# Performance work log

Hardware: AMD Instinct MI355X
Metric: run time of the kernel (lower is better)

## Reference

```python
import jax, jax.numpy as jnp
import numpy as np

# Circuit structure constants (HCLT-style tensorized probabilistic circuit)
V = 128      # num_vars
M = 256      # num_latents (input nodes per variable)
C = 64       # num categories per variable
B = 256      # batch size
L = 4        # number of inner (prod, sum) layer pairs
N = 32768    # sum nodes per inner layer
K = 4        # sum-node fanin (children product elements per sum node)
A = 2        # product-node arity
E = N * K    # product elements per layer
NUM_INPUT = V * M


def setup_inputs() -> dict:
    key = jax.random.key(0)
    k1, k2, k3, k4 = jax.random.split(key, 4)
    inputs = jax.random.randint(k1, (B, V), 0, C)                          # [B, V] categorical data
    input_logits = jax.random.normal(k2, (NUM_INPUT, C), dtype=jnp.float32)  # per input-node categorical logits
    sum_logits = jax.random.normal(k3, (L, N, K), dtype=jnp.float32)         # per sum-node edge logits (grouped softmax)
    root_logits = jax.random.normal(k4, (N,), dtype=jnp.float32)             # root sum-node edge logits
    # Irregular child index structure: prod element e in layer l gathers A children
    # from any node computed so far (dummy node 0 excluded, indices >= 1).
    rng = np.random.default_rng(0)
    base = 1 + NUM_INPUT
    child = np.stack([rng.integers(1, base + l * N, size=(E, A)) for l in range(L)], axis=0)
    prod_child_ids = jnp.asarray(child, dtype=jnp.int32)                    # [L, E, A]
    return {"inputs": inputs, "input_logits": input_logits, "sum_logits": sum_logits,
            "root_logits": root_logits, "prod_child_ids": prod_child_ids}


def reference(inputs, input_logits, sum_logits, root_logits, prod_child_ids):
    # --- input layer: node_mars for input nodes = log p(x_{vid(n)} | node n) ---
    logp = jax.nn.log_softmax(input_logits, axis=-1)            # [VM, C]
    vids = jnp.arange(NUM_INPUT) // M                           # variable id per input node
    cats = inputs[:, vids].T                                    # [VM, B] category index per (node, batch)
    in_mars = jnp.take_along_axis(logp, cats, axis=1)           # [VM, B]
    # node 0 is the dummy node with log-marginal 0.0 (as in the original buffer init)
    node_buf = jnp.concatenate([jnp.zeros((1, B), dtype=in_mars.dtype), in_mars], axis=0)
    # --- inner layers: alternating ProdLayer (gather+add) and SumLayer (softmax params + logsumexp) ---
    for l in range(L):
        ch = node_buf[prod_child_ids[l]]                        # [E, A, B] irregular gather
        elem = ch.sum(axis=1)                                   # element_mars: [E, B]
        logw = jax.nn.log_softmax(sum_logits[l], axis=-1)       # per-node grouped softmax: [N, K]
        nodes = jax.nn.logsumexp(elem.reshape(N, K, B) + logw[:, :, None], axis=1)  # [N, B]
        node_buf = jnp.concatenate([node_buf, nodes], axis=0)
    # --- root sum node ---
    rw = jax.nn.log_softmax(root_logits)                        # [N]
    lls = jax.nn.logsumexp(node_buf[-N:] + rw[:, None], axis=0) # [B]
    return lls[:, None]                                         # [B, num_roots=1]
```

## Files before the change

kernel.cpp:

```cpp
#include <hip/hip_runtime.h>
#include <math.h>

#define V 128
#define M 256
#define CAT 64
#define B 256
#define LAYERS 4
#define N 32768
#define K 4
#define AR 2
#define E (N * K)
#define NUM_INPUT (V * M)
#define BASE (1 + NUM_INPUT)
#define TOTAL_ROWS (BASE + LAYERS * N)
#define L3N 32
#define NPART (N / L3N)
#define R1BLK 32

typedef _Float16 half8 __attribute__((ext_vector_type(8)));
typedef _Float16 half4 __attribute__((ext_vector_type(4)));
typedef float float8_t __attribute__((ext_vector_type(8)));

#define OFF_IN 5.2f
__device__ __forceinline__ float layer_off(int l) {
    const float o[4] = {11.4f, 23.5f, 47.5f, 95.5f};
    return o[l];
}
__device__ __forceinline__ float row_off(int row) {
    return (row < BASE) ? OFF_IN : layer_off((row - BASE) >> 15);
}

__global__ __launch_bounds__(256) void input_layer_kernel(
    const int* __restrict__ inputs,
    const float* __restrict__ input_logits,
    _Float16* __restrict__ buf)
{
    __shared__ float lg[4][CAT];
    __shared__ int cats[B];
    __shared__ float lzs[4];
    const int t = threadIdx.x;
    const int n0 = blockIdx.x * 4;

    lg[t >> 6][t & 63] = input_logits[(size_t)n0 * CAT + t];
    cats[t] = inputs[t * V + (n0 >> 8)];
    __syncthreads();

    const int w = t >> 6;
    const int l = t & 63;
    float x = lg[w][l];
    float m = x;
    #pragma unroll
    for (int off = 32; off >= 1; off >>= 1) m = fmaxf(m, __shfl_xor(m, off));
    float s = __expf(x - m);
    #pragma unroll
    for (int off = 32; off >= 1; off >>= 1) s += __shfl_xor(s, off);
    if (l == 0) lzs[w] = m + __logf(s);
    __syncthreads();

    const float logZ = lzs[w];
    half4 r;
    #pragma unroll
    for (int j = 0; j < 4; ++j) {
        const int c = cats[4 * l + j];
        r[j] = (_Float16)(lg[w][c] - logZ + OFF_IN);
    }
    ((half4*)buf)[(size_t)(1 + n0 + w) * (B / 4) + l] = r;

    if (blockIdx.x == 0 && t < B / 4) {
        half4 z;
        z[0] = z[1] = z[2] = z[3] = (_Float16)OFF_IN;
        ((half4*)buf)[t] = z;
    }
}

__global__ __launch_bounds__(256) void layer_kernel(
    const int* __restrict__ child,
    const float* __restrict__ slog,
    _Float16* __restrict__ buf,
    int out_row0, int layer)
{
    __shared__ int ch[8][K * AR];
    __shared__ float w[8][K];
    const int t = threadIdx.x;
    const int i0 = blockIdx.x * 8;

    if (t < 64) ((int*)ch)[t] = child[(size_t)i0 * (K * AR) + t];
    __syncthreads();

    if (t < 32) {
        const float x = slog[(size_t)i0 * K + t];
        float mm = fmaxf(x, __shfl_xor(x, 1));
        mm = fmaxf(mm, __shfl_xor(mm, 2));
        float e = __expf(x - mm);
        float ss = e + __shfl_xor(e, 1);
        ss += __shfl_xor(ss, 2);
        const float lz = mm + __logf(ss);
        const int j = t >> 2, k = t & 3;
        w[j][k] = x - lz - row_off(ch[j][2 * k]) - row_off(ch[j][2 * k + 1])
                  + layer_off(layer);
    }
    __syncthreads();

    const int g = t >> 5;
    const int l = t & 31;
    const half8* bufv = (const half8*)buf;

    float8_t v[K];
    #pragma unroll
    for (int k = 0; k < K; ++k) {
        const half8 a = bufv[ch[g][2 * k]     * (B / 8) + l];
        const half8 b = bufv[ch[g][2 * k + 1] * (B / 8) + l];
        v[k] = __builtin_convertvector(a, float8_t) +
               __builtin_convertvector(b, float8_t) + w[g][k];
    }

    half8 r;
    #pragma unroll
    for (int j = 0; j < 8; ++j) {
        const float mm = fmaxf(fmaxf(v[0][j], v[1][j]), fmaxf(v[2][j], v[3][j]));
        const float ss = __expf(v[0][j] - mm) + __expf(v[1][j] - mm) +
                         __expf(v[2][j] - mm) + __expf(v[3][j] - mm);
        r[j] = (_Float16)(mm + __logf(ss));
    }
    ((half8*)buf)[(out_row0 + i0 + g) * (B / 8) + l] = r;
}

__global__ __launch_bounds__(1024) void layer3_root_kernel(
    const int* __restrict__ child,
    const float* __restrict__ slog,
    const _Float16* __restrict__ buf,
    const float* __restrict__ rlog,
    float* __restrict__ pm, float* __restrict__ ps)
{
    __shared__ int ch[L3N][K * AR];
    __shared__ float w[L3N][K];
    __shared__ float rl[L3N];
    __shared__ float vmat[B][L3N + 1];
    const int t = threadIdx.x;
    const int i0 = blockIdx.x * L3N;
    const float off3 = layer_off(3);

    if (t < L3N * 8) ((int*)ch)[t] = child[(size_t)i0 * (K * AR) + t];
    if (t >= 512 && t < 512 + L3N) rl[t - 512] = rlog[i0 + (t - 512)];
    __syncthreads();

    if (t < L3N * 4) {
        const float x = slog[(size_t)i0 * K + t];
        float mm = fmaxf(x, __shfl_xor(x, 1));
        mm = fmaxf(mm, __shfl_xor(mm, 2));
        float e = __expf(x - mm);
        float ss = e + __shfl_xor(e, 1);
        ss += __shfl_xor(ss, 2);
        const float lz = mm + __logf(ss);
        const int j = t >> 2, k = t & 3;
        w[j][k] = x - lz - row_off(ch[j][2 * k]) - row_off(ch[j][2 * k + 1])
                  + off3;
    }
    __syncthreads();

    const int g = t >> 5;
    const int l = t & 31;

    const half8* bufv = (const half8*)buf;
    float8_t v[K];
    #pragma unroll
    for (int k = 0; k < K; ++k) {
        const half8 a = bufv[ch[g][2 * k]     * (B / 8) + l];
        const half8 b = bufv[ch[g][2 * k + 1] * (B / 8) + l];
        v[k] = __builtin_convertvector(a, float8_t) +
               __builtin_convertvector(b, float8_t) + w[g][k];
    }

    const float radd = rl[g] - off3;
    #pragma unroll
    for (int j = 0; j < 8; ++j) {
        const float mm = fmaxf(fmaxf(v[0][j], v[1][j]), fmaxf(v[2][j], v[3][j]));
        const float ss = __expf(v[0][j] - mm) + __expf(v[1][j] - mm) +
                         __expf(v[2][j] - mm) + __expf(v[3][j] - mm);
        vmat[8 * l + j][g] = mm + __logf(ss) + radd;
    }
    __syncthreads();

    if (t < B) {
        float m = -INFINITY;
        #pragma unroll
        for (int q = 0; q < L3N; ++q) m = fmaxf(m, vmat[t][q]);
        float s = 0.0f;
        #pragma unroll
        for (int q = 0; q < L3N; ++q) s += __expf(vmat[t][q] - m);
        pm[blockIdx.x * B + t] = m;
        ps[blockIdx.x * B + t] = s;
    }
}

__global__ __launch_bounds__(256) void root_reduce1(
    const float* __restrict__ pm, const float* __restrict__ ps,
    float* __restrict__ pm2, float* __restrict__ ps2)
{
    const int j = blockIdx.x;
    const int c = threadIdx.x;
    const int Q = NPART / R1BLK;
    const int p0 = j * Q;

    float m = -INFINITY;
    #pragma unroll 8
    for (int q = 0; q < Q; ++q) m = fmaxf(m, pm[(p0 + q) * B + c]);
    float s = 0.0f;
    #pragma unroll 8
    for (int q = 0; q < Q; ++q)
        s += ps[(p0 + q) * B + c] * __expf(pm[(p0 + q) * B + c] - m);
    pm2[j * B + c] = m;
    ps2[j * B + c] = s;
}

__global__ __launch_bounds__(256) void root_combine_kernel(
    const float* __restrict__ rlog,
    const float* __restrict__ pm2, const float* __restrict__ ps2,
    float* __restrict__ out)
{
    __shared__ float red[256];
    const int t = threadIdx.x;

    float a0 = -INFINITY, a1 = -INFINITY, a2 = -INFINITY, a3 = -INFINITY;
    #pragma unroll 4
    for (int n = t; n < N; n += 1024) {
        a0 = fmaxf(a0, rlog[n]);
        a1 = fmaxf(a1, rlog[n + 256]);
        a2 = fmaxf(a2, rlog[n + 512]);
        a3 = fmaxf(a3, rlog[n + 768]);
    }
    red[t] = fmaxf(fmaxf(a0, a1), fmaxf(a2, a3));
    __syncthreads();
    for (int off = 128; off >= 1; off >>= 1) {
        if (t < off) red[t] = fmaxf(red[t], red[t + off]);
        __syncthreads();
    }
    const float gm = red[0];
    __syncthreads();

    float b0 = 0.f, b1 = 0.f, b2 = 0.f, b3 = 0.f;
    #pragma unroll 4
    for (int n = t; n < N; n += 1024) {
        b0 += __expf(rlog[n]       - gm);
        b1 += __expf(rlog[n + 256] - gm);
        b2 += __expf(rlog[n + 512] - gm);
        b3 += __expf(rlog[n + 768] - gm);
    }
    red[t] = (b0 + b1) + (b2 + b3);
    __syncthreads();
    for (int off = 128; off >= 1; off >>= 1) {
        if (t < off) red[t] += red[t + off];
        __syncthreads();
    }
    const float logZ = gm + __logf(red[0]);

    float m = -INFINITY;
    #pragma unroll 8
    for (int p = 0; p < R1BLK; ++p) m = fmaxf(m, pm2[p * B + t]);
    float s = 0.0f;
    #pragma unroll 8
    for (int p = 0; p < R1BLK; ++p)
        s += ps2[p * B + t] * __expf(pm2[p * B + t] - m);
    out[t] = m + __logf(s) - logZ;
}

extern "C" void kernel_launch(void* const* d_in, const int* in_sizes, int n_in,
                              void* d_out, int out_size, void* d_ws, size_t ws_size,
                              hipStream_t stream) {
    const int*   inputs       = (const int*)d_in[0];
    const float* input_logits = (const float*)d_in[1];
    const float* sum_logits   = (const float*)d_in[2];
    const float* root_logits  = (const float*)d_in[3];
    const int*   child        = (const int*)d_in[4];
    float* out = (float*)d_out;

    _Float16* buf = (_Float16*)d_ws;
    float* pm  = (float*)(buf + (size_t)TOTAL_ROWS * B);
    float* ps  = pm  + (size_t)NPART * B;
    float* pm2 = ps  + (size_t)NPART * B;
    float* ps2 = pm2 + (size_t)R1BLK * B;

    input_layer_kernel<<<NUM_INPUT / 4, 256, 0, stream>>>(inputs, input_logits, buf);

    for (int l = 0; l < LAYERS - 1; ++l) {
        layer_kernel<<<N / 8, 256, 0, stream>>>(
            child + (size_t)l * E * AR,
            sum_logits + (size_t)l * N * K,
            buf,
            BASE + l * N, l);
    }

    layer3_root_kernel<<<NPART, 1024, 0, stream>>>(
        child + (size_t)(LAYERS - 1) * E * AR,
        sum_logits + (size_t)(LAYERS - 1) * N * K,
        buf, root_logits, pm, ps);

    root_reduce1<<<R1BLK, 256, 0, stream>>>(pm, ps, pm2, ps2);
    root_combine_kernel<<<1, 256, 0, stream>>>(root_logits, pm2, ps2, out);
}
```

Measured before the change: 127.9 us.

## Rebuild input-node marginals on the fly from a compact log-prob table

The input stage no longer writes the full fp16 matrix of input-node marginals (one row per input node, times the batch). It now writes only a per-node fp16 log-softmax table (64 categories) and a byte-packed category matrix per variable. When a child index points to an input node, the layer kernels fetch the compact table row and the category bytes, then pick each batch element's value with a ds_bpermute lookup inside each 32-lane group. The aim is to cut the large input write and the 512-byte-per-row reads of input children. In exchange it adds branchy per-child decoding, cross-lane permute instructions and more registers in the gather kernels.

```diff
diff --git a/kernel.cpp b/kernel.cpp
--- a/kernel.cpp
+++ b/kernel.cpp
@@ -1,81 +1,104 @@
 #include <hip/hip_runtime.h>
 #include <math.h>
+#include <stdint.h>
 
 #define V 128
 #define M 256
 #define CAT 64
 #define B 256
 #define LAYERS 4
-#define N 32768
 #define K 4
 #define AR 2
-#define E (N * K)
+#define NNODES 32768
+#define E (NNODES * K)
 #define NUM_INPUT (V * M)
 #define BASE (1 + NUM_INPUT)
-#define TOTAL_ROWS (BASE + LAYERS * N)
+#define TOTAL_ROWS (BASE + LAYERS * NNODES)
 #define L3N 32
-#define NPART (N / L3N)
+#define NPART (NNODES / L3N)
 #define R1BLK 32
 
 typedef _Float16 half8 __attribute__((ext_vector_type(8)));
-typedef _Float16 half4 __attribute__((ext_vector_type(4)));
 typedef float float8_t __attribute__((ext_vector_type(8)));
 
 #define OFF_IN 5.2f
 __device__ __forceinline__ float layer_off(int l) {
-    const float o[4] = {11.4f, 23.5f, 47.5f, 95.5f};
-    return o[l];
+    return (l == 0) ? 11.4f : (l == 1) ? 23.5f : (l == 2) ? 47.5f : 95.5f;
 }
 __device__ __forceinline__ float row_off(int row) {
-    return (row < BASE) ? OFF_IN : layer_off((row - BASE) >> 15);
-}
-
-__global__ __launch_bounds__(256) void input_layer_kernel(
+    if (row < BASE) return OFF_IN;
+    return layer_off((row - BASE) >> 15);
+}
+
+__global__ __launch_bounds__(256) void input_prep_kernel(
     const int* __restrict__ inputs,
     const float* __restrict__ input_logits,
-    _Float16* __restrict__ buf)
-{
-    __shared__ float lg[4][CAT];
-    __shared__ int cats[B];
-    __shared__ float lzs[4];
+    _Float16* __restrict__ logp16,
+    unsigned char* __restrict__ cats)
+{
     const int t = threadIdx.x;
     const int n0 = blockIdx.x * 4;
-
-    lg[t >> 6][t & 63] = input_logits[(size_t)n0 * CAT + t];
-    cats[t] = inputs[t * V + (n0 >> 8)];
-    __syncthreads();
-
     const int w = t >> 6;
     const int l = t & 63;
-    float x = lg[w][l];
+    const int n = n0 + w;
+
+    const float x = input_logits[(size_t)n * CAT + l];
     float m = x;
     #pragma unroll
     for (int off = 32; off >= 1; off >>= 1) m = fmaxf(m, __shfl_xor(m, off));
     float s = __expf(x - m);
     #pragma unroll
     for (int off = 32; off >= 1; off >>= 1) s += __shfl_xor(s, off);
-    if (l == 0) lzs[w] = m + __logf(s);
-    __syncthreads();
-
-    const float logZ = lzs[w];
-    half4 r;
-    #pragma unroll
-    for (int j = 0; j < 4; ++j) {
-        const int c = cats[4 * l + j];
-        r[j] = (_Float16)(lg[w][c] - logZ + OFF_IN);
-    }
-    ((half4*)buf)[(size_t)(1 + n0 + w) * (B / 4) + l] = r;
-
-    if (blockIdx.x == 0 && t < B / 4) {
-        half4 z;
-        z[0] = z[1] = z[2] = z[3] = (_Float16)OFF_IN;
-        ((half4*)buf)[t] = z;
-    }
+    const float logZ = m + __logf(s);
+
+    logp16[(size_t)n * 64 + l] = (_Float16)(x - logZ + OFF_IN);
+
+    if ((blockIdx.x & 63) == 0) {
+        const int v = blockIdx.x >> 6;
+        cats[(size_t)v * B + t] = (unsigned char)inputs[t * V + v];
+    }
+}
+
+#define STAGE_CHILD(r, lane, bufq, lpu, catsu, S0, S1, S2, S3)                \
+    if ((r) >= BASE) {                                                        \
+        const uint4 q = (bufq)[(size_t)(r) * 32 + (lane)];                    \
+        S0 = q.x; S1 = q.y; S2 = q.z; S3 = q.w;                               \
+    } else {                                                                  \
+        const int nn_ = (r) - 1;                                              \
+        S0 = (lpu)[(size_t)nn_ * 32 + (lane)];                                \
+        const uint64_t cc_ = (catsu)[(size_t)(nn_ >> 8) * 32 + (lane)];       \
+        S1 = (uint32_t)cc_; S2 = (uint32_t)(cc_ >> 32); S3 = 0u;              \
+    }
+
+__device__ __forceinline__ float8_t finish_child(
+    int r, int phys, uint32_t s0, uint32_t s1, uint32_t s2, uint32_t s3)
+{
+    float8_t val;
+    if (r >= BASE) {
+        union { uint32_t u[4]; half8 hh; } q;
+        q.u[0] = s0; q.u[1] = s1; q.u[2] = s2; q.u[3] = s3;
+        val = __builtin_convertvector(q.hh, float8_t);
+    } else {
+        const uint32_t bl = (uint32_t)(phys & 32);
+        #pragma unroll
+        for (int j = 0; j < 8; ++j) {
+            const uint32_t cb = (((j < 4) ? s1 : s2) >> (8 * (j & 3))) & 63u;
+            const uint32_t got = (uint32_t)__builtin_amdgcn_ds_bpermute(
+                (int)(((cb >> 1) | bl) << 2), (int)s0);
+            const unsigned short hb = (cb & 1u) ? (unsigned short)(got >> 16)
+                                                : (unsigned short)(got & 0xffffu);
+            union { unsigned short u; _Float16 h; } cv; cv.u = hb;
+            val[j] = (float)cv.h;
+        }
+    }
+    return val;
 }
 
 __global__ __launch_bounds__(256) void layer_kernel(
     const int* __restrict__ child,
     const float* __restrict__ slog,
+    const _Float16* __restrict__ logp16,
+    const unsigned char* __restrict__ cats,
     _Float16* __restrict__ buf,
     int out_row0, int layer)
 {
@@ -101,33 +124,43 @@
     }
     __syncthreads();
 
-    const int g = t >> 5;
-    const int l = t & 31;
-    const half8* bufv = (const half8*)buf;
+    const int g = t >> 5, lane = t & 31, phys = t & 63;
+    const uint4* bufq = (const uint4*)buf;
+    const uint32_t* lpu = (const uint32_t*)logp16;
+    const uint64_t* catsu = (const uint64_t*)cats;
+
+    uint32_t s0[8], s1[8], s2[8], s3[8];
+    #pragma unroll
+    for (int c = 0; c < 8; ++c) {
+        const int r = ch[g][c];
+        STAGE_CHILD(r, lane, bufq, lpu, catsu, s0[c], s1[c], s2[c], s3[c]);
+    }
 
     float8_t v[K];
     #pragma unroll
     for (int k = 0; k < K; ++k) {
-        const half8 a = bufv[ch[g][2 * k]     * (B / 8) + l];
-        const half8 b = bufv[ch[g][2 * k + 1] * (B / 8) + l];
-        v[k] = __builtin_convertvector(a, float8_t) +
-               __builtin_convertvector(b, float8_t) + w[g][k];
-    }
-
-    half8 r;
+        const int c0 = 2 * k, c1 = 2 * k + 1;
+        const float8_t a = finish_child(ch[g][c0], phys, s0[c0], s1[c0], s2[c0], s3[c0]);
+        const float8_t b = finish_child(ch[g][c1], phys, s0[c1], s1[c1], s2[c1], s3[c1]);
+        v[k] = a + b + w[g][k];
+    }
+
+    half8 r8;
     #pragma unroll
     for (int j = 0; j < 8; ++j) {
         const float mm = fmaxf(fmaxf(v[0][j], v[1][j]), fmaxf(v[2][j], v[3][j]));
         const float ss = __expf(v[0][j] - mm) + __expf(v[1][j] - mm) +
                          __expf(v[2][j] - mm) + __expf(v[3][j] - mm);
-        r[j] = (_Float16)(mm + __logf(ss));
-    }
-    ((half8*)buf)[(out_row0 + i0 + g) * (B / 8) + l] = r;
+        r8[j] = (_Float16)(mm + __logf(ss));
+    }
+    ((half8*)buf)[(size_t)(out_row0 + i0 + g) * 32 + lane] = r8;
 }
 
 __global__ __launch_bounds__(1024) void layer3_root_kernel(
     const int* __restrict__ child,
     const float* __restrict__ slog,
+    const _Float16* __restrict__ logp16,
+    const unsigned char* __restrict__ cats,
     const _Float16* __restrict__ buf,
     const float* __restrict__ rlog,
     float* __restrict__ pm, float* __restrict__ ps)
@@ -158,17 +191,25 @@
     }
     __syncthreads();
 
-    const int g = t >> 5;
-    const int l = t & 31;
-
-    const half8* bufv = (const half8*)buf;
+    const int g = t >> 5, lane = t & 31, phys = t & 63;
+    const uint4* bufq = (const uint4*)buf;
+    const uint32_t* lpu = (const uint32_t*)logp16;
+    const uint64_t* catsu = (const uint64_t*)cats;
+
+    uint32_t s0[8], s1[8], s2[8], s3[8];
+    #pragma unroll
+    for (int c = 0; c < 8; ++c) {
+        const int r = ch[g][c];
+        STAGE_CHILD(r, lane, bufq, lpu, catsu, s0[c], s1[c], s2[c], s3[c]);
+    }
+
     float8_t v[K];
     #pragma unroll
     for (int k = 0; k < K; ++k) {
-        const half8 a = bufv[ch[g][2 * k]     * (B / 8) + l];
-        const half8 b = bufv[ch[g][2 * k + 1] * (B / 8) + l];
-        v[k] = __builtin_convertvector(a, float8_t) +
-               __builtin_convertvector(b, float8_t) + w[g][k];
+        const int c0 = 2 * k, c1 = 2 * k + 1;
+        const float8_t a = finish_child(ch[g][c0], phys, s0[c0], s1[c0], s2[c0], s3[c0]);
+        const float8_t b = finish_child(ch[g][c1], phys, s0[c1], s1[c1], s2[c1], s3[c1]);
+        v[k] = a + b + w[g][k];
     }
 
     const float radd = rl[g] - off3;
@@ -177,7 +218,7 @@
         const float mm = fmaxf(fmaxf(v[0][j], v[1][j]), fmaxf(v[2][j], v[3][j]));
         const float ss = __expf(v[0][j] - mm) + __expf(v[1][j] - mm) +
                          __expf(v[2][j] - mm) + __expf(v[3][j] - mm);
-        vmat[8 * l + j][g] = mm + __logf(ss) + radd;
+        vmat[8 * lane + j][g] = mm + __logf(ss) + radd;
     }
     __syncthreads();
 
@@ -223,7 +264,7 @@
 
     float a0 = -INFINITY, a1 = -INFINITY, a2 = -INFINITY, a3 = -INFINITY;
     #pragma unroll 4
-    for (int n = t; n < N; n += 1024) {
+    for (int n = t; n < NNODES; n += 1024) {
         a0 = fmaxf(a0, rlog[n]);
         a1 = fmaxf(a1, rlog[n + 256]);
         a2 = fmaxf(a2, rlog[n + 512]);
@@ -240,7 +281,7 @@
 
     float b0 = 0.f, b1 = 0.f, b2 = 0.f, b3 = 0.f;
     #pragma unroll 4
-    for (int n = t; n < N; n += 1024) {
+    for (int n = t; n < NNODES; n += 1024) {
         b0 += __expf(rlog[n]       - gm);
         b1 += __expf(rlog[n + 256] - gm);
         b2 += __expf(rlog[n + 512] - gm);
@@ -275,25 +316,27 @@
     float* out = (float*)d_out;
 
     _Float16* buf = (_Float16*)d_ws;
-    float* pm  = (float*)(buf + (size_t)TOTAL_ROWS * B);
+    _Float16* logp16 = buf + (size_t)TOTAL_ROWS * B;
+    unsigned char* cats = (unsigned char*)(logp16 + (size_t)NUM_INPUT * 64);
+    float* pm  = (float*)(cats + (size_t)V * B);
     float* ps  = pm  + (size_t)NPART * B;
     float* pm2 = ps  + (size_t)NPART * B;
     float* ps2 = pm2 + (size_t)R1BLK * B;
 
-    input_layer_kernel<<<NUM_INPUT / 4, 256, 0, stream>>>(inputs, input_logits, buf);
+    input_prep_kernel<<<NUM_INPUT / 4, 256, 0, stream>>>(inputs, input_logits,
+                                                         logp16, cats);
 
     for (int l = 0; l < LAYERS - 1; ++l) {
-        layer_kernel<<<N / 8, 256, 0, stream>>>(
+        layer_kernel<<<NNODES / 8, 256, 0, stream>>>(
             child + (size_t)l * E * AR,
-            sum_logits + (size_t)l * N * K,
-            buf,
-            BASE + l * N, l);
+            sum_logits + (size_t)l * NNODES * K,
+            logp16, cats, buf, BASE + l * NNODES, l);
     }
 
     layer3_root_kernel<<<NPART, 1024, 0, stream>>>(
         child + (size_t)(LAYERS - 1) * E * AR,
-        sum_logits + (size_t)(LAYERS - 1) * N * K,
-        buf, root_logits, pm, ps);
+        sum_logits + (size_t)(LAYERS - 1) * NNODES * K,
+        logp16, cats, buf, root_logits, pm, ps);
 
     root_reduce1<<<R1BLK, 256, 0, stream>>>(pm, ps, pm2, ps2);
     root_combine_kernel<<<1, 256, 0, stream>>>(root_logits, pm2, ps2, out);
```

Measured after the change: 171.1 us. 33.7% more time.

## Partition batch columns across XCDs so each die's L2 caches a node-buffer slice

Applied to the files above, without the earlier changes.

Layer kernels now split the 256-wide batch into eight 32-column slices and assign the slice by blockIdx&7, relying on round-robin dispatch of blocks to the eight XCDs. Each XCD then gathers only its own 64-byte slice of every child row, so its private L2 holds one eighth of the fp16 node buffer instead of the whole thing. Each block handles 32 nodes with 8 threads per node and issues all eight child loads up front. The root layer kernel is rewritten to match, with 256-thread blocks writing partial max/sum per 32-column slice. The gathers become narrower 8-byte loads, and the locality gain depends on the hardware keeping its block-to-XCD mapping.

```diff
diff --git a/kernel.cpp b/kernel.cpp
--- a/kernel.cpp
+++ b/kernel.cpp
@@ -1,33 +1,32 @@
 #include <hip/hip_runtime.h>
 #include <math.h>
+#include <stdint.h>
 
 #define V 128
 #define M 256
 #define CAT 64
 #define B 256
 #define LAYERS 4
-#define N 32768
 #define K 4
 #define AR 2
-#define E (N * K)
+#define NNODES 32768
+#define E (NNODES * K)
 #define NUM_INPUT (V * M)
 #define BASE (1 + NUM_INPUT)
-#define TOTAL_ROWS (BASE + LAYERS * N)
-#define L3N 32
-#define NPART (N / L3N)
+#define TOTAL_ROWS (BASE + LAYERS * NNODES)
+#define NPART 1024
 #define R1BLK 32
 
-typedef _Float16 half8 __attribute__((ext_vector_type(8)));
 typedef _Float16 half4 __attribute__((ext_vector_type(4)));
-typedef float float8_t __attribute__((ext_vector_type(8)));
+typedef float float4v __attribute__((ext_vector_type(4)));
 
 #define OFF_IN 5.2f
 __device__ __forceinline__ float layer_off(int l) {
-    const float o[4] = {11.4f, 23.5f, 47.5f, 95.5f};
-    return o[l];
+    return (l == 0) ? 11.4f : (l == 1) ? 23.5f : (l == 2) ? 47.5f : 95.5f;
 }
 __device__ __forceinline__ float row_off(int row) {
-    return (row < BASE) ? OFF_IN : layer_off((row - BASE) >> 15);
+    if (row < BASE) return OFF_IN;
+    return layer_off((row - BASE) >> 15);
 }
 
 __global__ __launch_bounds__(256) void input_layer_kernel(
@@ -73,21 +72,23 @@
     }
 }
 
-__global__ __launch_bounds__(256) void layer_kernel(
+__global__ __launch_bounds__(256) void layer_kernel_xcd(
     const int* __restrict__ child,
     const float* __restrict__ slog,
     _Float16* __restrict__ buf,
     int out_row0, int layer)
 {
-    __shared__ int ch[8][K * AR];
-    __shared__ float w[8][K];
+    __shared__ int ch[32][K * AR];
+    __shared__ float w[32][K];
     const int t = threadIdx.x;
-    const int i0 = blockIdx.x * 8;
-
-    if (t < 64) ((int*)ch)[t] = child[(size_t)i0 * (K * AR) + t];
-    __syncthreads();
-
-    if (t < 32) {
+    const int xcd = blockIdx.x & 7;
+    const int chunk = blockIdx.x >> 3;
+    const int i0 = chunk * 32;
+
+    ((int*)ch)[t] = child[(size_t)i0 * (K * AR) + t];
+    __syncthreads();
+
+    if (t < 128) {
         const float x = slog[(size_t)i0 * K + t];
         float mm = fmaxf(x, __shfl_xor(x, 1));
         mm = fmaxf(mm, __shfl_xor(mm, 2));
@@ -101,50 +102,57 @@
     }
     __syncthreads();
 
-    const int g = t >> 5;
-    const int l = t & 31;
-    const half8* bufv = (const half8*)buf;
-
-    float8_t v[K];
+    const int g = t >> 3;
+    const int s = t & 7;
+    const int off = xcd * 8 + s;
+    const uint2* bufu = (const uint2*)buf;
+
+    uint2 st[8];
+    #pragma unroll
+    for (int c = 0; c < 8; ++c)
+        st[c] = bufu[(size_t)ch[g][c] * 64 + off];
+
+    float4v v[K];
     #pragma unroll
     for (int k = 0; k < K; ++k) {
-        const half8 a = bufv[ch[g][2 * k]     * (B / 8) + l];
-        const half8 b = bufv[ch[g][2 * k + 1] * (B / 8) + l];
-        v[k] = __builtin_convertvector(a, float8_t) +
-               __builtin_convertvector(b, float8_t) + w[g][k];
-    }
-
-    half8 r;
-    #pragma unroll
-    for (int j = 0; j < 8; ++j) {
+        union { uint2 u; half4 h; } ua, ub;
+        ua.u = st[2 * k]; ub.u = st[2 * k + 1];
+        v[k] = __builtin_convertvector(ua.h, float4v) +
+               __builtin_convertvector(ub.h, float4v) + w[g][k];
+    }
+
+    union { uint2 u; half4 h; } ro;
+    #pragma unroll
+    for (int j = 0; j < 4; ++j) {
         const float mm = fmaxf(fmaxf(v[0][j], v[1][j]), fmaxf(v[2][j], v[3][j]));
         const float ss = __expf(v[0][j] - mm) + __expf(v[1][j] - mm) +
                          __expf(v[2][j] - mm) + __expf(v[3][j] - mm);
-        r[j] = (_Float16)(mm + __logf(ss));
-    }
-    ((half8*)buf)[(out_row0 + i0 + g) * (B / 8) + l] = r;
-}
-
-__global__ __launch_bounds__(1024) void layer3_root_kernel(
+        ro.h[j] = (_Float16)(mm + __logf(ss));
+    }
+    ((uint2*)buf)[(size_t)(out_row0 + i0 + g) * 64 + off] = ro.u;
+}
+
+__global__ __launch_bounds__(256) void layer3_root_xcd(
     const int* __restrict__ child,
     const float* __restrict__ slog,
     const _Float16* __restrict__ buf,
     const float* __restrict__ rlog,
     float* __restrict__ pm, float* __restrict__ ps)
 {
-    __shared__ int ch[L3N][K * AR];
-    __shared__ float w[L3N][K];
-    __shared__ float rl[L3N];
-    __shared__ float vmat[B][L3N + 1];
+    __shared__ int ch[32][K * AR];
+    __shared__ float w[32][K];
+    __shared__ float rl[32];
+    __shared__ float vmat[32][33];
     const int t = threadIdx.x;
-    const int i0 = blockIdx.x * L3N;
+    const int xcd = blockIdx.x & 7;
+    const int chunk = blockIdx.x >> 3;
+    const int i0 = chunk * 32;
     const float off3 = layer_off(3);
 
-    if (t < L3N * 8) ((int*)ch)[t] = child[(size_t)i0 * (K * AR) + t];
-    if (t >= 512 && t < 512 + L3N) rl[t - 512] = rlog[i0 + (t - 512)];
-    __syncthreads();
-
-    if (t < L3N * 4) {
+    ((int*)ch)[t] = child[(size_t)i0 * (K * AR) + t];
+    __syncthreads();
+
+    if (t < 128) {
         const float x = slog[(size_t)i0 * K + t];
         float mm = fmaxf(x, __shfl_xor(x, 1));
         mm = fmaxf(mm, __shfl_xor(mm, 2));
@@ -155,41 +163,49 @@
         const int j = t >> 2, k = t & 3;
         w[j][k] = x - lz - row_off(ch[j][2 * k]) - row_off(ch[j][2 * k + 1])
                   + off3;
-    }
-    __syncthreads();
-
-    const int g = t >> 5;
-    const int l = t & 31;
-
-    const half8* bufv = (const half8*)buf;
-    float8_t v[K];
+    } else if (t < 160) {
+        rl[t - 128] = rlog[i0 + (t - 128)];
+    }
+    __syncthreads();
+
+    const int g = t >> 3;
+    const int s = t & 7;
+    const int off = xcd * 8 + s;
+    const uint2* bufu = (const uint2*)buf;
+
+    uint2 st[8];
+    #pragma unroll
+    for (int c = 0; c < 8; ++c)
+        st[c] = bufu[(size_t)ch[g][c] * 64 + off];
+
+    float4v v[K];
     #pragma unroll
     for (int k = 0; k < K; ++k) {
-        const half8 a = bufv[ch[g][2 * k]     * (B / 8) + l];
-        const half8 b = bufv[ch[g][2 * k + 1] * (B / 8) + l];
-        v[k] = __builtin_convertvector(a, float8_t) +
-               __builtin_convertvector(b, float8_t) + w[g][k];
+        union { uint2 u; half4 h; } ua, ub;
+        ua.u = st[2 * k]; ub.u = st[2 * k + 1];
+        v[k] = __builtin_convertvector(ua.h, float4v) +
+               __builtin_convertvector(ub.h, float4v) + w[g][k];
     }
 
     const float radd = rl[g] - off3;
     #pragma unroll
-    for (int j = 0; j < 8; ++j) {
+    for (int j = 0; j < 4; ++j) {
         const float mm = fmaxf(fmaxf(v[0][j], v[1][j]), fmaxf(v[2][j], v[3][j]));
         const float ss = __expf(v[0][j] - mm) + __expf(v[1][j] - mm) +
                          __expf(v[2][j] - mm) + __expf(v[3][j] - mm);
-        vmat[8 * l + j][g] = mm + __logf(ss) + radd;
-    }
-    __syncthreads();
-
-    if (t < B) {
+        vmat[s * 4 + j][g] = mm + __logf(ss) + radd;
+    }
+    __syncthreads();
+
+    if (t < 32) {
         float m = -INFINITY;
         #pragma unroll
-        for (int q = 0; q < L3N; ++q) m = fmaxf(m, vmat[t][q]);
-        float s = 0.0f;
+        for (int q = 0; q < 32; ++q) m = fmaxf(m, vmat[t][q]);
+        float sum = 0.0f;
         #pragma unroll
-        for (int q = 0; q < L3N; ++q) s += __expf(vmat[t][q] - m);
-        pm[blockIdx.x * B + t] = m;
-        ps[blockIdx.x * B + t] = s;
+        for (int q = 0; q < 32; ++q) sum += __expf(vmat[t][q] - m);
+        pm[chunk * B + xcd * 32 + t] = m;
+        ps[chunk * B + xcd * 32 + t] = sum;
     }
 }
 
@@ -223,7 +239,7 @@
 
     float a0 = -INFINITY, a1 = -INFINITY, a2 = -INFINITY, a3 = -INFINITY;
     #pragma unroll 4
-    for (int n = t; n < N; n += 1024) {
+    for (int n = t; n < NNODES; n += 1024) {
         a0 = fmaxf(a0, rlog[n]);
         a1 = fmaxf(a1, rlog[n + 256]);
         a2 = fmaxf(a2, rlog[n + 512]);
@@ -240,7 +256,7 @@
 
     float b0 = 0.f, b1 = 0.f, b2 = 0.f, b3 = 0.f;
     #pragma unroll 4
-    for (int n = t; n < N; n += 1024) {
+    for (int n = t; n < NNODES; n += 1024) {
         b0 += __expf(rlog[n]       - gm);
         b1 += __expf(rlog[n + 256] - gm);
         b2 += __expf(rlog[n + 512] - gm);
@@ -283,16 +299,15 @@
     input_layer_kernel<<<NUM_INPUT / 4, 256, 0, stream>>>(inputs, input_logits, buf);
 
     for (int l = 0; l < LAYERS - 1; ++l) {
-        layer_kernel<<<N / 8, 256, 0, stream>>>(
+        layer_kernel_xcd<<<8 * NPART, 256, 0, stream>>>(
             child + (size_t)l * E * AR,
-            sum_logits + (size_t)l * N * K,
-            buf,
-            BASE + l * N, l);
-    }
-
-    layer3_root_kernel<<<NPART, 1024, 0, stream>>>(
+            sum_logits + (size_t)l * NNODES * K,
+            buf, BASE + l * NNODES, l);
+    }
+
+    layer3_root_xcd<<<8 * NPART, 256, 0, stream>>>(
         child + (size_t)(LAYERS - 1) * E * AR,
-        sum_logits + (size_t)(LAYERS - 1) * N * K,
+        sum_logits + (size_t)(LAYERS - 1) * NNODES * K,
         buf, root_logits, pm, ps);
 
     root_reduce1<<<R1BLK, 256, 0, stream>>>(pm, ps, pm2, ps2);
```

New measurement: 163.2 us. +27.5%, slower.
